# Optimization experiments

Hardware: AMD Instinct MI355X
Metric: run time of the kernel (lower is better)

The kernel has to match this reference:

```python
import jax, jax.numpy as jnp
import numpy as np
from jax import lax

B, L = 2, 1024
D_MODEL, D_STATE, EXPAND, D_CONV = 1024, 16, 2, 4
D_INNER = EXPAND * D_MODEL            # 2048
DT_RANK = (D_MODEL + 15) // 16        # 64


def setup_inputs() -> dict:
    key = jax.random.key(0)
    ks = jax.random.split(key, 8)
    g = lambda k, shape, s=0.02: jax.random.normal(k, shape, dtype=jnp.float32) * s
    # Mamba-style A init: A = -exp(A_log), A_log = log(1..d_state) per channel
    A_log = jnp.log(jnp.broadcast_to(
        jnp.arange(1, D_STATE + 1, dtype=jnp.float32), (D_INNER, D_STATE)))
    return {
        "x": jax.random.normal(ks[0], (B, L, D_MODEL), dtype=jnp.float32),
        "W_in": g(ks[1], (D_MODEL, 2 * D_INNER)),
        "conv_w": g(ks[2], (D_INNER, D_CONV), 0.1),
        "conv_b": jnp.zeros((D_INNER,), jnp.float32),
        "W_x": g(ks[3], (D_INNER, DT_RANK + 2 * D_STATE)),
        "W_dt": g(ks[4], (DT_RANK, D_INNER)),
        "b_dt": g(ks[5], (D_INNER,), 0.1),
        "A_log": A_log,
        "D_skip": jnp.ones((D_INNER,), jnp.float32),
        "W_out": g(ks[6], (D_INNER, D_MODEL)),
    }


def reference(x, W_in, conv_w, conv_b, W_x, W_dt, b_dt, A_log, D_skip, W_out):
    # in_proj -> (u, z): [B, L, D_INNER] each
    xz = x @ W_in
    u, z = xz[..., :D_INNER], xz[..., D_INNER:]

    # causal depthwise conv1d, kernel D_CONV (small fixed loop over taps)
    up = jnp.pad(u, ((0, 0), (D_CONV - 1, 0), (0, 0)))
    u = sum(up[:, k:k + L, :] * conv_w[:, k] for k in range(D_CONV)) + conv_b
    u = jax.nn.silu(u)

    # input-dependent dt, B, C
    x_dbl = u @ W_x                                    # [B, L, dt_rank + 2N]
    dt = x_dbl[..., :DT_RANK]
    Bm = x_dbl[..., DT_RANK:DT_RANK + D_STATE]         # [B, L, N]
    Cm = x_dbl[..., DT_RANK + D_STATE:]                # [B, L, N]
    delta = jax.nn.softplus(dt @ W_dt + b_dt)          # [B, L, D]

    A = -jnp.exp(A_log)                                # [D, N]
    deltaA = jnp.exp(jnp.einsum('bld,dn->bldn', delta, A))   # [B, L, D, N]
    dBu = (delta * u)[..., None] * Bm[:, :, None, :]          # [B, L, D, N]

    def step(h, inp):
        dA_t, dBu_t, c_t = inp                         # [B,D,N],[B,D,N],[B,N]
        h = dA_t * h + dBu_t
        y_t = jnp.einsum('bdn,bn->bd', h, c_t)
        return h, y_t

    h0 = jnp.zeros((B, D_INNER, D_STATE), x.dtype)
    _, ys = lax.scan(step, h0,
                     (deltaA.transpose(1, 0, 2, 3),
                      dBu.transpose(1, 0, 2, 3),
                      Cm.transpose(1, 0, 2)))
    y = ys.transpose(1, 0, 2) + u * D_skip             # [B, L, D_INNER]
    y = y * jax.nn.silu(z)                             # gated output
    return y @ W_out                                   # [B, L, D_MODEL]
```

## Files before the change

### kernel.cpp

```cpp
#include <hip/hip_runtime.h>


typedef unsigned short u16;
typedef unsigned int   u32;

#define B_SZ 2
#define L_SZ 1024
#define DM   1024
#define DI   2048
#define DS   16
#define DTR  64
#define NXD  96
#define NCHUNK 32
#define CL   32
#define KSPLIT 8
#define KC     256

typedef __bf16 bf16x8 __attribute__((ext_vector_type(8)));
typedef float  f32x4  __attribute__((ext_vector_type(4)));

__device__ __forceinline__ u16 f2bf(float f) {
    u32 x = __float_as_uint(f);
    x += 0x7fffu + ((x >> 16) & 1u);
    return (u16)(x >> 16);
}
__device__ __forceinline__ float bf2f(u16 v) {
    return __uint_as_float(((u32)v) << 16);
}

__device__ __forceinline__ void gld_lds16(const u16* g, u16* l) {
    __builtin_amdgcn_global_load_lds(
        (const __attribute__((address_space(1))) u32*)g,
        (__attribute__((address_space(3))) u32*)l, 16, 0, 0);
}

__device__ __forceinline__ void wg_barrier() {
    __asm__ volatile("" ::: "memory");
    __builtin_amdgcn_s_barrier();
    __asm__ volatile("" ::: "memory");
}
#define WAIT_VM12() __builtin_amdgcn_s_waitcnt(0xF7C)
#define WAIT_VM9()  __builtin_amdgcn_s_waitcnt(0xF79)
#define WAIT_VM8()  __builtin_amdgcn_s_waitcnt(0xF78)
#define WAIT_VM6()  __builtin_amdgcn_s_waitcnt(0xF76)
#define WAIT_VM4()  __builtin_amdgcn_s_waitcnt(0xF74)
#define WAIT_VM3()  __builtin_amdgcn_s_waitcnt(0xF73)
#define WAIT_VM0()  __builtin_amdgcn_s_waitcnt(0xF70)

__global__ __launch_bounds__(256) void gemm128p(
    const u16* __restrict__ A, const u16* __restrict__ BT,
    float* __restrict__ Cf, u16* __restrict__ Cb,
    int M, int N, int K, int op)
{
    __shared__ u16 As[4][128 * 32];
    __shared__ u16 Bs[4][128 * 32];

    const int tid  = threadIdx.x;
    const int wave = tid >> 6;
    const int lane = tid & 63;
    const int q    = lane >> 4;
    const int r16  = lane & 15;
    const int wm   = (wave & 1) * 64;
    const int wn   = (wave >> 1) * 64;
    const int m0   = blockIdx.y * 128;
    const int n0   = blockIdx.x * 128;

    const u16* gA0 = A  + (size_t)(m0 + (tid >> 2))      * K + (tid & 3) * 8;
    const u16* gA1 = A  + (size_t)(m0 + 64 + (tid >> 2)) * K + (tid & 3) * 8;
    const u16* gB0 = BT + (size_t)(n0 + (tid >> 2))      * K + (tid & 3) * 8;
    const u16* gB1 = BT + (size_t)(n0 + 64 + (tid >> 2)) * K + (tid & 3) * 8;

    const int niter = K >> 5;
    const int pre = niter < 3 ? niter : 3;
    for (int p = 0; p < pre; ++p) {
        const int k0 = p * 32;
        gld_lds16(gA0 + k0, &As[p][tid * 8]);
        gld_lds16(gA1 + k0, &As[p][2048 + tid * 8]);
        gld_lds16(gB0 + k0, &Bs[p][tid * 8]);
        gld_lds16(gB1 + k0, &Bs[p][2048 + tid * 8]);
    }

    f32x4 acc[4][4];
#pragma unroll
    for (int s = 0; s < 4; ++s)
#pragma unroll
        for (int j = 0; j < 4; ++j) acc[s][j] = (f32x4){0.f, 0.f, 0.f, 0.f};

    for (int it = 0; it < niter; ++it) {
        if (it + 3 < niter) {
            const int k0 = (it + 3) * 32;
            const int bi = (it + 3) & 3;
            gld_lds16(gA0 + k0, &As[bi][tid * 8]);
            gld_lds16(gA1 + k0, &As[bi][2048 + tid * 8]);
            gld_lds16(gB0 + k0, &Bs[bi][tid * 8]);
            gld_lds16(gB1 + k0, &Bs[bi][2048 + tid * 8]);
            WAIT_VM12();
        } else if (it + 2 < niter) {
            WAIT_VM8();
        } else if (it + 1 < niter) {
            WAIT_VM4();
        } else {
            WAIT_VM0();
        }
        wg_barrier();

        const int cur = it & 3;
        bf16x8 af[4], bfr[4];
#pragma unroll
        for (int s = 0; s < 4; ++s)
            af[s] = *(const bf16x8*)(&As[cur][(wm + s * 16 + r16) * 32 + q * 8]);
#pragma unroll
        for (int j = 0; j < 4; ++j)
            bfr[j] = *(const bf16x8*)(&Bs[cur][(wn + j * 16 + r16) * 32 + q * 8]);
#pragma unroll
        for (int s = 0; s < 4; ++s)
#pragma unroll
            for (int j = 0; j < 4; ++j)
                acc[s][j] = __builtin_amdgcn_mfma_f32_16x16x32_bf16(
                    af[s], bfr[j], acc[s][j], 0, 0, 0);

        wg_barrier();
    }

#pragma unroll
    for (int s = 0; s < 4; ++s) {
        const int row0 = m0 + wm + s * 16 + q * 4;
#pragma unroll
        for (int j = 0; j < 4; ++j) {
            const int col = n0 + wn + j * 16 + r16;
            if (op == 2) {
#pragma unroll
                for (int i = 0; i < 4; ++i)
                    Cb[(size_t)(row0 + i) * N + col] = f2bf(acc[s][j][i]);
            } else {
#pragma unroll
                for (int i = 0; i < 4; ++i)
                    Cf[(size_t)(row0 + i) * N + col] = acc[s][j][i];
            }
        }
    }
}

__global__ __launch_bounds__(256) void gemm_out64(
    const u16* __restrict__ A, const u16* __restrict__ BT,
    float* __restrict__ C, int M, int N, int K)
{
    __shared__ u16 As[4][128 * 32];
    __shared__ u16 Bs[4][64 * 32];

    const int tid  = threadIdx.x;
    const int wave = tid >> 6;
    const int lane = tid & 63;
    const int q    = lane >> 4;
    const int r16  = lane & 15;
    const int wm   = (wave & 1) * 64;
    const int wn   = (wave >> 1) * 32;
    const int m0   = blockIdx.y * 128;
    const int n0   = blockIdx.x * 64;

    const u16* gA0 = A  + (size_t)(m0 + (tid >> 2))      * K + (tid & 3) * 8;
    const u16* gA1 = A  + (size_t)(m0 + 64 + (tid >> 2)) * K + (tid & 3) * 8;
    const u16* gB0 = BT + (size_t)(n0 + (tid >> 2))      * K + (tid & 3) * 8;

    const int niter = K >> 5;
    const int pre = niter < 3 ? niter : 3;
    for (int p = 0; p < pre; ++p) {
        const int k0 = p * 32;
        gld_lds16(gA0 + k0, &As[p][tid * 8]);
        gld_lds16(gA1 + k0, &As[p][2048 + tid * 8]);
        gld_lds16(gB0 + k0, &Bs[p][tid * 8]);
    }

    f32x4 acc[4][2];
#pragma unroll
    for (int s = 0; s < 4; ++s)
#pragma unroll
        for (int j = 0; j < 2; ++j) acc[s][j] = (f32x4){0.f, 0.f, 0.f, 0.f};

    for (int it = 0; it < niter; ++it) {
        if (it + 3 < niter) {
            const int k0 = (it + 3) * 32;
            const int bi = (it + 3) & 3;
            gld_lds16(gA0 + k0, &As[bi][tid * 8]);
            gld_lds16(gA1 + k0, &As[bi][2048 + tid * 8]);
            gld_lds16(gB0 + k0, &Bs[bi][tid * 8]);
            WAIT_VM9();
        } else if (it + 2 < niter) {
            WAIT_VM6();
        } else if (it + 1 < niter) {
            WAIT_VM3();
        } else {
            WAIT_VM0();
        }
        wg_barrier();

        const int cur = it & 3;
        bf16x8 af[4], bfr[2];
#pragma unroll
        for (int s = 0; s < 4; ++s)
            af[s] = *(const bf16x8*)(&As[cur][(wm + s * 16 + r16) * 32 + q * 8]);
#pragma unroll
        for (int j = 0; j < 2; ++j)
            bfr[j] = *(const bf16x8*)(&Bs[cur][(wn + j * 16 + r16) * 32 + q * 8]);
#pragma unroll
        for (int s = 0; s < 4; ++s)
#pragma unroll
            for (int j = 0; j < 2; ++j)
                acc[s][j] = __builtin_amdgcn_mfma_f32_16x16x32_bf16(
                    af[s], bfr[j], acc[s][j], 0, 0, 0);

        wg_barrier();
    }

#pragma unroll
    for (int s = 0; s < 4; ++s) {
        const int row0 = m0 + wm + s * 16 + q * 4;
#pragma unroll
        for (int j = 0; j < 2; ++j) {
            const int col = n0 + wn + j * 16 + r16;
#pragma unroll
            for (int i = 0; i < 4; ++i)
                C[(size_t)(row0 + i) * N + col] = acc[s][j][i];
        }
    }
}

__global__ __launch_bounds__(256) void gemm_skinny_atomic(
    const u16* __restrict__ A, const u16* __restrict__ BT,
    float* xdbl, int M, int N, int K)
{
    constexpr int LDT = 40;
    __shared__ u16 As[128 * LDT];
    __shared__ u16 Bs[64 * LDT];

    const int tid  = threadIdx.x;
    const int wave = tid >> 6;
    const int lane = tid & 63;
    const int q    = lane >> 4;
    const int r16  = lane & 15;
    const int m0   = blockIdx.y * 128;
    const int n0   = blockIdx.x * 64;
    const int kcs  = blockIdx.z * KC;
    const int sr   = tid >> 2;
    const int ss   = (tid & 3) * 8;

    f32x4 acc[2][4];
#pragma unroll
    for (int s = 0; s < 2; ++s)
#pragma unroll
        for (int j = 0; j < 4; ++j) acc[s][j] = (f32x4){0.f, 0.f, 0.f, 0.f};

    const int bcol  = n0 + sr;
    const int bcolc = bcol < N ? bcol : N - 1;

    constexpr int NIT = KC / 32;
    uint4 a0 = *(const uint4*)(A + (size_t)(m0 + sr)      * K + kcs + ss);
    uint4 a1 = *(const uint4*)(A + (size_t)(m0 + 64 + sr) * K + kcs + ss);
    uint4 bv = *(const uint4*)(BT + (size_t)bcolc * K + kcs + ss);

    for (int it = 0; it < NIT; ++it) {
        wg_barrier();
        *(uint4*)(As + sr * LDT + ss)        = a0;
        *(uint4*)(As + (64 + sr) * LDT + ss) = a1;
        *(uint4*)(Bs + sr * LDT + ss)        = bv;
        const int kn = (it + 1 < NIT) ? (kcs + (it + 1) * 32) : kcs;
        a0 = *(const uint4*)(A + (size_t)(m0 + sr)      * K + kn + ss);
        a1 = *(const uint4*)(A + (size_t)(m0 + 64 + sr) * K + kn + ss);
        bv = *(const uint4*)(BT + (size_t)bcolc * K + kn + ss);
        __builtin_amdgcn_s_waitcnt(0xF70 | 0x0000);
        __builtin_amdgcn_s_waitcnt(0x070F);
        wg_barrier();

        bf16x8 af[2], bfr[4];
#pragma unroll
        for (int s = 0; s < 2; ++s)
            af[s] = *(const bf16x8*)(As + (wave * 32 + s * 16 + r16) * LDT + q * 8);
#pragma unroll
        for (int j = 0; j < 4; ++j)
            bfr[j] = *(const bf16x8*)(Bs + (j * 16 + r16) * LDT + q * 8);
#pragma unroll
        for (int s = 0; s < 2; ++s)
#pragma unroll
            for (int j = 0; j < 4; ++j)
                acc[s][j] = __builtin_amdgcn_mfma_f32_16x16x32_bf16(
                    af[s], bfr[j], acc[s][j], 0, 0, 0);
    }

#pragma unroll
    for (int s = 0; s < 2; ++s) {
        const int row0 = m0 + wave * 32 + s * 16 + q * 4;
#pragma unroll
        for (int j = 0; j < 4; ++j) {
            const int col = n0 + j * 16 + r16;
            if (col < N) {
#pragma unroll
                for (int i = 0; i < 4; ++i)
                    atomicAdd(&xdbl[(size_t)(row0 + i) * N + col], acc[s][j][i]);
            }
        }
    }
}

__global__ __launch_bounds__(256) void gemm_delta(
    const float* __restrict__ xdbl, const u16* __restrict__ BT,
    const float* __restrict__ bias, float* __restrict__ dlt)
{
    constexpr int LDT = 40;
    __shared__ u16 As[128 * LDT];
    __shared__ u16 Bs[128 * LDT];

    const int tid  = threadIdx.x;
    const int wave = tid >> 6;
    const int lane = tid & 63;
    const int q    = lane >> 4;
    const int r16  = lane & 15;
    const int wm   = (wave & 1) * 64;
    const int wn   = (wave >> 1) * 64;
    const int m0   = blockIdx.y * 128;
    const int n0   = blockIdx.x * 128;
    const int sr   = tid >> 2;
    const int ss   = (tid & 3) * 8;

    f32x4 acc[4][4];
#pragma unroll
    for (int s = 0; s < 4; ++s)
#pragma unroll
        for (int j = 0; j < 4; ++j) acc[s][j] = (f32x4){0.f, 0.f, 0.f, 0.f};

    for (int k0 = 0; k0 < DTR; k0 += 32) {
        __syncthreads();
        f32x4 f0 = *(const f32x4*)(xdbl + (size_t)(m0 + sr) * NXD + k0 + ss);
        f32x4 f1 = *(const f32x4*)(xdbl + (size_t)(m0 + sr) * NXD + k0 + ss + 4);
        f32x4 f2 = *(const f32x4*)(xdbl + (size_t)(m0 + 64 + sr) * NXD + k0 + ss);
        f32x4 f3 = *(const f32x4*)(xdbl + (size_t)(m0 + 64 + sr) * NXD + k0 + ss + 4);
        uint4 bv0 = *(const uint4*)(BT + (size_t)(n0 + sr)      * DTR + k0 + ss);
        uint4 bv1 = *(const uint4*)(BT + (size_t)(n0 + 64 + sr) * DTR + k0 + ss);
        u16* pa0 = As + sr * LDT + ss;
        u16* pa1 = As + (64 + sr) * LDT + ss;
#pragma unroll
        for (int i = 0; i < 4; ++i) { pa0[i] = f2bf(f0[i]); pa0[4 + i] = f2bf(f1[i]); }
#pragma unroll
        for (int i = 0; i < 4; ++i) { pa1[i] = f2bf(f2[i]); pa1[4 + i] = f2bf(f3[i]); }
        *(uint4*)(Bs + sr * LDT + ss)        = bv0;
        *(uint4*)(Bs + (64 + sr) * LDT + ss) = bv1;
        __syncthreads();

        bf16x8 af[4], bfr[4];
#pragma unroll
        for (int s = 0; s < 4; ++s)
            af[s] = *(const bf16x8*)(As + (wm + s * 16 + r16) * LDT + q * 8);
#pragma unroll
        for (int j = 0; j < 4; ++j)
            bfr[j] = *(const bf16x8*)(Bs + (wn + j * 16 + r16) * LDT + q * 8);
#pragma unroll
        for (int s = 0; s < 4; ++s)
#pragma unroll
            for (int j = 0; j < 4; ++j)
                acc[s][j] = __builtin_amdgcn_mfma_f32_16x16x32_bf16(
                    af[s], bfr[j], acc[s][j], 0, 0, 0);
    }

#pragma unroll
    for (int s = 0; s < 4; ++s) {
        const int row0 = m0 + wm + s * 16 + q * 4;
#pragma unroll
        for (int j = 0; j < 4; ++j) {
            const int col = n0 + wn + j * 16 + r16;
            const float bv = bias[col];
#pragma unroll
            for (int i = 0; i < 4; ++i) {
                float v = acc[s][j][i] + bv;
                v = (v > 20.f) ? v : log1pf(__expf(v));
                dlt[(size_t)(row0 + i) * DI + col] = v;
            }
        }
    }
}

__device__ __forceinline__ void tr_tile(
    const float* __restrict__ in, u16* __restrict__ out,
    int R, int C, int tr, int tc, int tid, float (*t)[33])
{
    const int tx = tid & 31, ty = tid >> 5;
    const int r0 = tr * 32, c0 = tc * 32;
#pragma unroll
    for (int i = 0; i < 4; ++i) {
        int r = r0 + ty + i * 8, c = c0 + tx;
        if (r < R && c < C) t[ty + i * 8][tx] = in[(size_t)r * C + c];
    }
    __syncthreads();
#pragma unroll
    for (int i = 0; i < 4; ++i) {
        int oR = c0 + ty + i * 8, oC = r0 + tx;
        if (oR < C && oC < R) out[(size_t)oR * R + oC] = f2bf(t[tx][ty + i * 8]);
    }
}

__global__ __launch_bounds__(256) void prep_kernel(
    const float* __restrict__ x,     u16* __restrict__ xbf,
    const float* __restrict__ W_in,  u16* __restrict__ winT,
    const float* __restrict__ W_out, u16* __restrict__ woutT,
    const float* __restrict__ W_x,   u16* __restrict__ wxT,
    const float* __restrict__ W_dt,  u16* __restrict__ wdtT,
    float* __restrict__ xdbl)
{
    __shared__ float t[32][33];
    const int id  = blockIdx.x;
    const int tid = threadIdx.x;
    if (id < 4096) {
        tr_tile(W_in, winT, 1024, 4096, id >> 7, id & 127, tid, t);
    } else if (id < 6144) {
        int i2 = id - 4096;
        tr_tile(W_out, woutT, 2048, 1024, i2 >> 5, i2 & 31, tid, t);
    } else if (id < 6336) {
        int i3 = id - 6144;
        tr_tile(W_x, wxT, 2048, 96, i3 / 3, i3 % 3, tid, t);
    } else if (id < 6464) {
        int i4 = id - 6336;
        tr_tile(W_dt, wdtT, 64, 2048, i4 >> 6, i4 & 63, tid, t);
    } else if (id < 14656) {
        int i = (id - 6464) * 256 + tid;
        xbf[i] = f2bf(x[i]);
    } else {
        f32x4 z = (f32x4){0.f, 0.f, 0.f, 0.f};
        ((f32x4*)xdbl)[(size_t)(id - 14656) * 256 + tid] = z;
    }
}

__global__ __launch_bounds__(256) void conv_silu_kernel(
    const u16* __restrict__ xzbf, const float* __restrict__ cw,
    const float* __restrict__ cb, u16* __restrict__ ucbf)
{
    const int idx = blockIdx.x * 256 + threadIdx.x;
    const int d   = idx & (DI - 1);
    const int pos = idx >> 11;
    const int l   = pos & (L_SZ - 1);
    float s = cb[d];
#pragma unroll
    for (int k = 0; k < 4; ++k) {
        int ls = l + k - 3;
        if (ls >= 0)
            s = fmaf(bf2f(xzbf[(size_t)(pos + k - 3) * (2 * DI) + d]), cw[d * 4 + k], s);
    }
    float v = s / (1.f + __expf(-s));
    ucbf[idx] = f2bf(v);
}

__global__ __launch_bounds__(256) void scan_pass1(
    const float* __restrict__ delta, const u16* __restrict__ ucbf,
    const float* __restrict__ xdbl, const float* __restrict__ A_log,
    float* __restrict__ hbuf, float* __restrict__ pbuf)
{
    const int c = blockIdx.x;
    const int d = blockIdx.y * 256 + threadIdx.x;
    const int b = blockIdx.z;
    float Av[16], h[16], P[16];
#pragma unroll
    for (int n = 0; n < 16; ++n) {
        Av[n] = -__expf(A_log[d * 16 + n]);
        h[n] = 0.f; P[n] = 1.f;
    }
    const int rowbase = b * L_SZ + c * CL;
    for (int i = 0; i < CL; ++i) {
        const int row = rowbase + i;
        float dlt = delta[(size_t)row * DI + d];
        float uu  = bf2f(ucbf[(size_t)row * DI + d]);
        float du  = dlt * uu;
        const float* xr = xdbl + (size_t)row * NXD;
#pragma unroll
        for (int n = 0; n < 16; ++n) {
            float e = __expf(dlt * Av[n]);
            P[n] *= e;
            h[n] = fmaf(e, h[n], du * xr[DTR + n]);
        }
    }
    size_t base = ((size_t)((b * NCHUNK + c) * DI + d)) * 16;
#pragma unroll
    for (int n = 0; n < 16; ++n) { hbuf[base + n] = h[n]; pbuf[base + n] = P[n]; }
}

__global__ __launch_bounds__(256) void scan_pass2(
    float* __restrict__ hbuf, const float* __restrict__ pbuf)
{
    const int j = blockIdx.x * 256 + threadIdx.x;
    const int b = blockIdx.y;
    float h0 = 0.f;
    for (int cc = 0; cc < NCHUNK; ++cc) {
        size_t o = ((size_t)(b * NCHUNK + cc)) * (DI * 16) + j;
        float hl = hbuf[o];
        float Pl = pbuf[o];
        hbuf[o] = h0;
        h0 = fmaf(Pl, h0, hl);
    }
}

__global__ __launch_bounds__(256) void scan_pass3(
    const float* __restrict__ delta, const u16* __restrict__ ucbf,
    const float* __restrict__ xdbl, const float* __restrict__ A_log,
    const float* __restrict__ hbuf, const u16* __restrict__ xzbf,
    const float* __restrict__ Dskip, u16* __restrict__ ybf)
{
    const int c = blockIdx.x;
    const int d = blockIdx.y * 256 + threadIdx.x;
    const int b = blockIdx.z;
    float Av[16], h[16];
    size_t base = ((size_t)((b * NCHUNK + c) * DI + d)) * 16;
#pragma unroll
    for (int n = 0; n < 16; ++n) {
        Av[n] = -__expf(A_log[d * 16 + n]);
        h[n]  = hbuf[base + n];
    }
    const float Dk = Dskip[d];
    const int rowbase = b * L_SZ + c * CL;
    for (int i = 0; i < CL; ++i) {
        const int row = rowbase + i;
        float dlt = delta[(size_t)row * DI + d];
        float uu  = bf2f(ucbf[(size_t)row * DI + d]);
        float du  = dlt * uu;
        const float* xr = xdbl + (size_t)row * NXD;
        float y = 0.f;
#pragma unroll
        for (int n = 0; n < 16; ++n) {
            float e = __expf(dlt * Av[n]);
            h[n] = fmaf(e, h[n], du * xr[DTR + n]);
            y = fmaf(h[n], xr[DTR + DS + n], y);
        }
        float zz = bf2f(xzbf[(size_t)row * (2 * DI) + DI + d]);
        float yv = fmaf(uu, Dk, y) * (zz / (1.f + __expf(-zz)));
        ybf[(size_t)row * DI + d] = f2bf(yv);
    }
}

constexpr size_t OFF_DELTA   = 0;
constexpr size_t OFF_XDBL    = OFF_DELTA + 4194304;
constexpr size_t OFF_HBUF    = OFF_XDBL  + 196608;
constexpr size_t OFF_PBUF    = OFF_HBUF  + 2097152;
constexpr size_t OFF_F32_END = OFF_PBUF  + 2097152;
constexpr size_t SOFF_XBF   = 0;
constexpr size_t SOFF_WINT  = SOFF_XBF   + 2097152;
constexpr size_t SOFF_XZBF  = SOFF_WINT  + 4194304;
constexpr size_t SOFF_UCBF  = SOFF_XZBF  + 8388608;
constexpr size_t SOFF_WXT   = SOFF_UCBF  + 4194304;
constexpr size_t SOFF_WDTT  = SOFF_WXT   + 196608;
constexpr size_t SOFF_WOUTT = SOFF_WDTT  + 131072;
constexpr size_t SOFF_YBF   = SOFF_WOUTT + 2097152;

extern "C" void kernel_launch(void* const* d_in, const int* in_sizes, int n_in,
                              void* d_out, int out_size, void* d_ws, size_t ws_size,
                              hipStream_t stream)
{
    const float* x     = (const float*)d_in[0];
    const float* W_in  = (const float*)d_in[1];
    const float* cw    = (const float*)d_in[2];
    const float* cb    = (const float*)d_in[3];
    const float* W_x   = (const float*)d_in[4];
    const float* W_dt  = (const float*)d_in[5];
    const float* b_dt  = (const float*)d_in[6];
    const float* A_log = (const float*)d_in[7];
    const float* Dsk   = (const float*)d_in[8];
    const float* W_out = (const float*)d_in[9];
    float* out = (float*)d_out;

    float* wsf   = (float*)d_ws;
    float* dlt   = wsf + OFF_DELTA;
    float* xdbl  = wsf + OFF_XDBL;
    float* hbuf  = wsf + OFF_HBUF;
    float* pbuf  = wsf + OFF_PBUF;
    u16* sb    = (u16*)(wsf + OFF_F32_END);
    u16* xbf   = sb + SOFF_XBF;
    u16* winT  = sb + SOFF_WINT;
    u16* xzbf  = sb + SOFF_XZBF;
    u16* ucbf  = sb + SOFF_UCBF;
    u16* wxT   = sb + SOFF_WXT;
    u16* wdtT  = sb + SOFF_WDTT;
    u16* woutT = sb + SOFF_WOUTT;
    u16* ybf   = sb + SOFF_YBF;

    prep_kernel<<<14848, 256, 0, stream>>>(x, xbf, W_in, winT, W_out, woutT,
                                           W_x, wxT, W_dt, wdtT, xdbl);

    gemm128p<<<dim3(32, 16), 256, 0, stream>>>(
        xbf, winT, nullptr, xzbf, 2048, 4096, 1024, 2);

    conv_silu_kernel<<<(B_SZ * L_SZ * DI) / 256, 256, 0, stream>>>(xzbf, cw, cb, ucbf);

    gemm_skinny_atomic<<<dim3(2, 16, KSPLIT), 256, 0, stream>>>(
        ucbf, wxT, xdbl, 2048, NXD, 2048);

    gemm_delta<<<dim3(16, 16), 256, 0, stream>>>(xdbl, wdtT, b_dt, dlt);

    scan_pass1<<<dim3(NCHUNK, DI / 256, B_SZ), 256, 0, stream>>>(dlt, ucbf, xdbl, A_log, hbuf, pbuf);
    scan_pass2<<<dim3(DI * 16 / 256, B_SZ), 256, 0, stream>>>(hbuf, pbuf);
    scan_pass3<<<dim3(NCHUNK, DI / 256, B_SZ), 256, 0, stream>>>(dlt, ucbf, xdbl, A_log, hbuf, xzbf, Dsk, ybf);

    gemm_out64<<<dim3(16, 16), 256, 0, stream>>>(ybf, woutT, out, 2048, 1024, 2048);
}
```

Measured before the change: 262.9 us.

## Fuse conv, x-proj, delta GEMM and three scan passes into one cooperative kernel

```diff
diff --git a/kernel.cpp b/kernel.cpp
--- a/kernel.cpp
+++ b/kernel.cpp
@@ -1,5 +1,8 @@
 #include <hip/hip_runtime.h>
-
+#include <hip/hip_cooperative_groups.h>
+
+
+namespace cg = cooperative_groups;
 
 typedef unsigned short u16;
 typedef unsigned int   u32;
@@ -46,6 +49,7 @@
 #define WAIT_VM4()  __builtin_amdgcn_s_waitcnt(0xF74)
 #define WAIT_VM3()  __builtin_amdgcn_s_waitcnt(0xF73)
 #define WAIT_VM0()  __builtin_amdgcn_s_waitcnt(0xF70)
+#define WAIT_LGKM0() __builtin_amdgcn_s_waitcnt(0x070F)
 
 __global__ __launch_bounds__(256) void gemm128p(
     const u16* __restrict__ A, const u16* __restrict__ BT,
@@ -221,158 +225,6 @@
 #pragma unroll
             for (int i = 0; i < 4; ++i)
                 C[(size_t)(row0 + i) * N + col] = acc[s][j][i];
-        }
-    }
-}
-
-__global__ __launch_bounds__(256) void gemm_skinny_atomic(
-    const u16* __restrict__ A, const u16* __restrict__ BT,
-    float* xdbl, int M, int N, int K)
-{
-    constexpr int LDT = 40;
-    __shared__ u16 As[128 * LDT];
-    __shared__ u16 Bs[64 * LDT];
-
-    const int tid  = threadIdx.x;
-    const int wave = tid >> 6;
-    const int lane = tid & 63;
-    const int q    = lane >> 4;
-    const int r16  = lane & 15;
-    const int m0   = blockIdx.y * 128;
-    const int n0   = blockIdx.x * 64;
-    const int kcs  = blockIdx.z * KC;
-    const int sr   = tid >> 2;
-    const int ss   = (tid & 3) * 8;
-
-    f32x4 acc[2][4];
-#pragma unroll
-    for (int s = 0; s < 2; ++s)
-#pragma unroll
-        for (int j = 0; j < 4; ++j) acc[s][j] = (f32x4){0.f, 0.f, 0.f, 0.f};
-
-    const int bcol  = n0 + sr;
-    const int bcolc = bcol < N ? bcol : N - 1;
-
-    constexpr int NIT = KC / 32;
-    uint4 a0 = *(const uint4*)(A + (size_t)(m0 + sr)      * K + kcs + ss);
-    uint4 a1 = *(const uint4*)(A + (size_t)(m0 + 64 + sr) * K + kcs + ss);
-    uint4 bv = *(const uint4*)(BT + (size_t)bcolc * K + kcs + ss);
-
-    for (int it = 0; it < NIT; ++it) {
-        wg_barrier();
-        *(uint4*)(As + sr * LDT + ss)        = a0;
-        *(uint4*)(As + (64 + sr) * LDT + ss) = a1;
-        *(uint4*)(Bs + sr * LDT + ss)        = bv;
-        const int kn = (it + 1 < NIT) ? (kcs + (it + 1) * 32) : kcs;
-        a0 = *(const uint4*)(A + (size_t)(m0 + sr)      * K + kn + ss);
-        a1 = *(const uint4*)(A + (size_t)(m0 + 64 + sr) * K + kn + ss);
-        bv = *(const uint4*)(BT + (size_t)bcolc * K + kn + ss);
-        __builtin_amdgcn_s_waitcnt(0xF70 | 0x0000);
-        __builtin_amdgcn_s_waitcnt(0x070F);
-        wg_barrier();
-
-        bf16x8 af[2], bfr[4];
-#pragma unroll
-        for (int s = 0; s < 2; ++s)
-            af[s] = *(const bf16x8*)(As + (wave * 32 + s * 16 + r16) * LDT + q * 8);
-#pragma unroll
-        for (int j = 0; j < 4; ++j)
-            bfr[j] = *(const bf16x8*)(Bs + (j * 16 + r16) * LDT + q * 8);
-#pragma unroll
-        for (int s = 0; s < 2; ++s)
-#pragma unroll
-            for (int j = 0; j < 4; ++j)
-                acc[s][j] = __builtin_amdgcn_mfma_f32_16x16x32_bf16(
-                    af[s], bfr[j], acc[s][j], 0, 0, 0);
-    }
-
-#pragma unroll
-    for (int s = 0; s < 2; ++s) {
-        const int row0 = m0 + wave * 32 + s * 16 + q * 4;
-#pragma unroll
-        for (int j = 0; j < 4; ++j) {
-            const int col = n0 + j * 16 + r16;
-            if (col < N) {
-#pragma unroll
-                for (int i = 0; i < 4; ++i)
-                    atomicAdd(&xdbl[(size_t)(row0 + i) * N + col], acc[s][j][i]);
-            }
-        }
-    }
-}
-
-__global__ __launch_bounds__(256) void gemm_delta(
-    const float* __restrict__ xdbl, const u16* __restrict__ BT,
-    const float* __restrict__ bias, float* __restrict__ dlt)
-{
-    constexpr int LDT = 40;
-    __shared__ u16 As[128 * LDT];
-    __shared__ u16 Bs[128 * LDT];
-
-    const int tid  = threadIdx.x;
-    const int wave = tid >> 6;
-    const int lane = tid & 63;
-    const int q    = lane >> 4;
-    const int r16  = lane & 15;
-    const int wm   = (wave & 1) * 64;
-    const int wn   = (wave >> 1) * 64;
-    const int m0   = blockIdx.y * 128;
-    const int n0   = blockIdx.x * 128;
-    const int sr   = tid >> 2;
-    const int ss   = (tid & 3) * 8;
-
-    f32x4 acc[4][4];
-#pragma unroll
-    for (int s = 0; s < 4; ++s)
-#pragma unroll
-        for (int j = 0; j < 4; ++j) acc[s][j] = (f32x4){0.f, 0.f, 0.f, 0.f};
-
-    for (int k0 = 0; k0 < DTR; k0 += 32) {
-        __syncthreads();
-        f32x4 f0 = *(const f32x4*)(xdbl + (size_t)(m0 + sr) * NXD + k0 + ss);
-        f32x4 f1 = *(const f32x4*)(xdbl + (size_t)(m0 + sr) * NXD + k0 + ss + 4);
-        f32x4 f2 = *(const f32x4*)(xdbl + (size_t)(m0 + 64 + sr) * NXD + k0 + ss);
-        f32x4 f3 = *(const f32x4*)(xdbl + (size_t)(m0 + 64 + sr) * NXD + k0 + ss + 4);
-        uint4 bv0 = *(const uint4*)(BT + (size_t)(n0 + sr)      * DTR + k0 + ss);
-        uint4 bv1 = *(const uint4*)(BT + (size_t)(n0 + 64 + sr) * DTR + k0 + ss);
-        u16* pa0 = As + sr * LDT + ss;
-        u16* pa1 = As + (64 + sr) * LDT + ss;
-#pragma unroll
-        for (int i = 0; i < 4; ++i) { pa0[i] = f2bf(f0[i]); pa0[4 + i] = f2bf(f1[i]); }
-#pragma unroll
-        for (int i = 0; i < 4; ++i) { pa1[i] = f2bf(f2[i]); pa1[4 + i] = f2bf(f3[i]); }
-        *(uint4*)(Bs + sr * LDT + ss)        = bv0;
-        *(uint4*)(Bs + (64 + sr) * LDT + ss) = bv1;
-        __syncthreads();
-
-        bf16x8 af[4], bfr[4];
-#pragma unroll
-        for (int s = 0; s < 4; ++s)
-            af[s] = *(const bf16x8*)(As + (wm + s * 16 + r16) * LDT + q * 8);
-#pragma unroll
-        for (int j = 0; j < 4; ++j)
-            bfr[j] = *(const bf16x8*)(Bs + (wn + j * 16 + r16) * LDT + q * 8);
-#pragma unroll
-        for (int s = 0; s < 4; ++s)
-#pragma unroll
-            for (int j = 0; j < 4; ++j)
-                acc[s][j] = __builtin_amdgcn_mfma_f32_16x16x32_bf16(
-                    af[s], bfr[j], acc[s][j], 0, 0, 0);
-    }
-
-#pragma unroll
-    for (int s = 0; s < 4; ++s) {
-        const int row0 = m0 + wm + s * 16 + q * 4;
-#pragma unroll
-        for (int j = 0; j < 4; ++j) {
-            const int col = n0 + wn + j * 16 + r16;
-            const float bv = bias[col];
-#pragma unroll
-            for (int i = 0; i < 4; ++i) {
-                float v = acc[s][j][i] + bv;
-                v = (v > 20.f) ? v : log1pf(__expf(v));
-                dlt[(size_t)(row0 + i) * DI + col] = v;
-            }
         }
     }
 }
@@ -427,107 +279,249 @@
     }
 }
 
-__global__ __launch_bounds__(256) void conv_silu_kernel(
+__global__ __launch_bounds__(256, 2) void mega_kernel(
     const u16* __restrict__ xzbf, const float* __restrict__ cw,
-    const float* __restrict__ cb, u16* __restrict__ ucbf)
+    const float* __restrict__ cb, u16* __restrict__ ucbf,
+    const u16* __restrict__ wxT, float* __restrict__ xdbl,
+    const u16* __restrict__ wdtT, const float* __restrict__ b_dt,
+    float* __restrict__ dlt,
+    const float* __restrict__ A_log, const float* __restrict__ Dsk,
+    float* __restrict__ hbuf, float* __restrict__ pbuf,
+    u16* __restrict__ ybf)
 {
-    const int idx = blockIdx.x * 256 + threadIdx.x;
-    const int d   = idx & (DI - 1);
-    const int pos = idx >> 11;
-    const int l   = pos & (L_SZ - 1);
-    float s = cb[d];
-#pragma unroll
-    for (int k = 0; k < 4; ++k) {
-        int ls = l + k - 3;
-        if (ls >= 0)
-            s = fmaf(bf2f(xzbf[(size_t)(pos + k - 3) * (2 * DI) + d]), cw[d * 4 + k], s);
-    }
-    float v = s / (1.f + __expf(-s));
-    ucbf[idx] = f2bf(v);
-}
-
-__global__ __launch_bounds__(256) void scan_pass1(
-    const float* __restrict__ delta, const u16* __restrict__ ucbf,
-    const float* __restrict__ xdbl, const float* __restrict__ A_log,
-    float* __restrict__ hbuf, float* __restrict__ pbuf)
-{
-    const int c = blockIdx.x;
-    const int d = blockIdx.y * 256 + threadIdx.x;
-    const int b = blockIdx.z;
-    float Av[16], h[16], P[16];
-#pragma unroll
-    for (int n = 0; n < 16; ++n) {
-        Av[n] = -__expf(A_log[d * 16 + n]);
-        h[n] = 0.f; P[n] = 1.f;
-    }
-    const int rowbase = b * L_SZ + c * CL;
-    for (int i = 0; i < CL; ++i) {
-        const int row = rowbase + i;
-        float dlt = delta[(size_t)row * DI + d];
-        float uu  = bf2f(ucbf[(size_t)row * DI + d]);
-        float du  = dlt * uu;
-        const float* xr = xdbl + (size_t)row * NXD;
+    cg::grid_group grid = cg::this_grid();
+    const int bid = blockIdx.x;
+    const int tid = threadIdx.x;
+
+    constexpr int LDT = 40;
+    __shared__ u16 As[128 * LDT];
+    __shared__ u16 Bs[64 * LDT];
+
+    for (int idx = bid * 256 + tid; idx < B_SZ * L_SZ * DI; idx += 512 * 256) {
+        const int d   = idx & (DI - 1);
+        const int pos = idx >> 11;
+        const int l   = pos & (L_SZ - 1);
+        float s = cb[d];
+#pragma unroll
+        for (int k = 0; k < 4; ++k) {
+            int ls = l + k - 3;
+            if (ls >= 0)
+                s = fmaf(bf2f(xzbf[(size_t)(pos + k - 3) * (2 * DI) + d]), cw[d * 4 + k], s);
+        }
+        float v = s / (1.f + __expf(-s));
+        ucbf[idx] = f2bf(v);
+    }
+    grid.sync();
+
+    if (bid < 256) {
+        const int wave = tid >> 6, lane = tid & 63;
+        const int q = lane >> 4, r16 = lane & 15;
+        const int n0  = (bid & 1) * 64;
+        const int m0  = ((bid >> 1) & 15) * 128;
+        const int kcs = (bid >> 5) * KC;
+        const int sr  = tid >> 2, ss = (tid & 3) * 8;
+
+        f32x4 acc[2][4];
+#pragma unroll
+        for (int s = 0; s < 2; ++s)
+#pragma unroll
+            for (int j = 0; j < 4; ++j) acc[s][j] = (f32x4){0.f, 0.f, 0.f, 0.f};
+
+        const int bcol  = n0 + sr;
+        const int bcolc = bcol < NXD ? bcol : NXD - 1;
+
+        constexpr int NIT = KC / 32;
+        uint4 a0 = *(const uint4*)(ucbf + (size_t)(m0 + sr)      * DI + kcs + ss);
+        uint4 a1 = *(const uint4*)(ucbf + (size_t)(m0 + 64 + sr) * DI + kcs + ss);
+        uint4 bv = *(const uint4*)(wxT + (size_t)bcolc * DI + kcs + ss);
+
+        for (int it = 0; it < NIT; ++it) {
+            wg_barrier();
+            *(uint4*)(As + sr * LDT + ss)        = a0;
+            *(uint4*)(As + (64 + sr) * LDT + ss) = a1;
+            *(uint4*)(Bs + sr * LDT + ss)        = bv;
+            const int kn = (it + 1 < NIT) ? (kcs + (it + 1) * 32) : kcs;
+            a0 = *(const uint4*)(ucbf + (size_t)(m0 + sr)      * DI + kn + ss);
+            a1 = *(const uint4*)(ucbf + (size_t)(m0 + 64 + sr) * DI + kn + ss);
+            bv = *(const uint4*)(wxT + (size_t)bcolc * DI + kn + ss);
+            WAIT_LGKM0();
+            wg_barrier();
+
+            bf16x8 af[2], bfr[4];
+#pragma unroll
+            for (int s = 0; s < 2; ++s)
+                af[s] = *(const bf16x8*)(As + (wave * 32 + s * 16 + r16) * LDT + q * 8);
+#pragma unroll
+            for (int j = 0; j < 4; ++j)
+                bfr[j] = *(const bf16x8*)(Bs + (j * 16 + r16) * LDT + q * 8);
+#pragma unroll
+            for (int s = 0; s < 2; ++s)
+#pragma unroll
+                for (int j = 0; j < 4; ++j)
+                    acc[s][j] = __builtin_amdgcn_mfma_f32_16x16x32_bf16(
+                        af[s], bfr[j], acc[s][j], 0, 0, 0);
+        }
+
+#pragma unroll
+        for (int s = 0; s < 2; ++s) {
+            const int row0 = m0 + wave * 32 + s * 16 + q * 4;
+#pragma unroll
+            for (int j = 0; j < 4; ++j) {
+                const int col = n0 + j * 16 + r16;
+                if (col < NXD) {
+#pragma unroll
+                    for (int i = 0; i < 4; ++i)
+                        atomicAdd(&xdbl[(size_t)(row0 + i) * NXD + col], acc[s][j][i]);
+                }
+            }
+        }
+    }
+    grid.sync();
+
+    {
+        const int wave = tid >> 6, lane = tid & 63;
+        const int q = lane >> 4, r16 = lane & 15;
+        const int wm = (wave & 1) * 64, wn = (wave >> 1) * 32;
+        const int n0 = (bid & 31) * 64;
+        const int m0 = (bid >> 5) * 128;
+        const int sr = tid >> 2, ss = (tid & 3) * 8;
+
+        f32x4 acc[4][2];
+#pragma unroll
+        for (int s = 0; s < 4; ++s)
+#pragma unroll
+            for (int j = 0; j < 2; ++j) acc[s][j] = (f32x4){0.f, 0.f, 0.f, 0.f};
+
+        for (int k0 = 0; k0 < DTR; k0 += 32) {
+            __syncthreads();
+            f32x4 f0 = *(const f32x4*)(xdbl + (size_t)(m0 + sr) * NXD + k0 + ss);
+            f32x4 f1 = *(const f32x4*)(xdbl + (size_t)(m0 + sr) * NXD + k0 + ss + 4);
+            f32x4 f2 = *(const f32x4*)(xdbl + (size_t)(m0 + 64 + sr) * NXD + k0 + ss);
+            f32x4 f3 = *(const f32x4*)(xdbl + (size_t)(m0 + 64 + sr) * NXD + k0 + ss + 4);
+            uint4 bv0 = *(const uint4*)(wdtT + (size_t)(n0 + sr) * DTR + k0 + ss);
+            u16* pa0 = As + sr * LDT + ss;
+            u16* pa1 = As + (64 + sr) * LDT + ss;
+#pragma unroll
+            for (int i = 0; i < 4; ++i) { pa0[i] = f2bf(f0[i]); pa0[4 + i] = f2bf(f1[i]); }
+#pragma unroll
+            for (int i = 0; i < 4; ++i) { pa1[i] = f2bf(f2[i]); pa1[4 + i] = f2bf(f3[i]); }
+            *(uint4*)(Bs + sr * LDT + ss) = bv0;
+            __syncthreads();
+
+            bf16x8 af[4], bfr[2];
+#pragma unroll
+            for (int s = 0; s < 4; ++s)
+                af[s] = *(const bf16x8*)(As + (wm + s * 16 + r16) * LDT + q * 8);
+#pragma unroll
+            for (int j = 0; j < 2; ++j)
+                bfr[j] = *(const bf16x8*)(Bs + (wn + j * 16 + r16) * LDT + q * 8);
+#pragma unroll
+            for (int s = 0; s < 4; ++s)
+#pragma unroll
+                for (int j = 0; j < 2; ++j)
+                    acc[s][j] = __builtin_amdgcn_mfma_f32_16x16x32_bf16(
+                        af[s], bfr[j], acc[s][j], 0, 0, 0);
+        }
+
+#pragma unroll
+        for (int s = 0; s < 4; ++s) {
+            const int row0 = m0 + wm + s * 16 + q * 4;
+#pragma unroll
+            for (int j = 0; j < 2; ++j) {
+                const int col = n0 + wn + j * 16 + r16;
+                const float bv = b_dt[col];
+#pragma unroll
+                for (int i = 0; i < 4; ++i) {
+                    float v = acc[s][j][i] + bv;
+                    v = (v > 20.f) ? v : log1pf(__expf(v));
+                    dlt[(size_t)(row0 + i) * DI + col] = v;
+                }
+            }
+        }
+    }
+    grid.sync();
+
+    {
+        const int c = bid & 31;
+        const int r = bid >> 5;
+        const int g = r & 7;
+        const int b = r >> 3;
+        const int d = g * 256 + tid;
+        float Av[16], h[16], P[16];
 #pragma unroll
         for (int n = 0; n < 16; ++n) {
-            float e = __expf(dlt * Av[n]);
-            P[n] *= e;
-            h[n] = fmaf(e, h[n], du * xr[DTR + n]);
-        }
-    }
-    size_t base = ((size_t)((b * NCHUNK + c) * DI + d)) * 16;
-#pragma unroll
-    for (int n = 0; n < 16; ++n) { hbuf[base + n] = h[n]; pbuf[base + n] = P[n]; }
-}
-
-__global__ __launch_bounds__(256) void scan_pass2(
-    float* __restrict__ hbuf, const float* __restrict__ pbuf)
-{
-    const int j = blockIdx.x * 256 + threadIdx.x;
-    const int b = blockIdx.y;
-    float h0 = 0.f;
-    for (int cc = 0; cc < NCHUNK; ++cc) {
-        size_t o = ((size_t)(b * NCHUNK + cc)) * (DI * 16) + j;
-        float hl = hbuf[o];
-        float Pl = pbuf[o];
-        hbuf[o] = h0;
-        h0 = fmaf(Pl, h0, hl);
-    }
-}
-
-__global__ __launch_bounds__(256) void scan_pass3(
-    const float* __restrict__ delta, const u16* __restrict__ ucbf,
-    const float* __restrict__ xdbl, const float* __restrict__ A_log,
-    const float* __restrict__ hbuf, const u16* __restrict__ xzbf,
-    const float* __restrict__ Dskip, u16* __restrict__ ybf)
-{
-    const int c = blockIdx.x;
-    const int d = blockIdx.y * 256 + threadIdx.x;
-    const int b = blockIdx.z;
-    float Av[16], h[16];
-    size_t base = ((size_t)((b * NCHUNK + c) * DI + d)) * 16;
-#pragma unroll
-    for (int n = 0; n < 16; ++n) {
-        Av[n] = -__expf(A_log[d * 16 + n]);
-        h[n]  = hbuf[base + n];
-    }
-    const float Dk = Dskip[d];
-    const int rowbase = b * L_SZ + c * CL;
-    for (int i = 0; i < CL; ++i) {
-        const int row = rowbase + i;
-        float dlt = delta[(size_t)row * DI + d];
-        float uu  = bf2f(ucbf[(size_t)row * DI + d]);
-        float du  = dlt * uu;
-        const float* xr = xdbl + (size_t)row * NXD;
-        float y = 0.f;
+            Av[n] = -__expf(A_log[d * 16 + n]);
+            h[n] = 0.f; P[n] = 1.f;
+        }
+        const int rowbase = b * L_SZ + c * CL;
+        for (int i = 0; i < CL; ++i) {
+            const int row = rowbase + i;
+            float dv = dlt[(size_t)row * DI + d];
+            float uu = bf2f(ucbf[(size_t)row * DI + d]);
+            float du = dv * uu;
+            const float* xr = xdbl + (size_t)row * NXD;
+#pragma unroll
+            for (int n = 0; n < 16; ++n) {
+                float e = __expf(dv * Av[n]);
+                P[n] *= e;
+                h[n] = fmaf(e, h[n], du * xr[DTR + n]);
+            }
+        }
+        size_t base = ((size_t)((b * NCHUNK + c) * DI + d)) * 16;
+#pragma unroll
+        for (int n = 0; n < 16; ++n) { hbuf[base + n] = h[n]; pbuf[base + n] = P[n]; }
+    }
+    grid.sync();
+
+    {
+        const int tidg = bid * 256 + tid;
+        if (tidg < 2 * DI * 16) {
+            const int b = tidg >> 15;
+            const int j = tidg & (DI * 16 - 1);
+            float h0 = 0.f;
+            for (int cc = 0; cc < NCHUNK; ++cc) {
+                size_t o = ((size_t)(b * NCHUNK + cc)) * (DI * 16) + j;
+                float hl = hbuf[o];
+                float Pl = pbuf[o];
+                hbuf[o] = h0;
+                h0 = fmaf(Pl, h0, hl);
+            }
+        }
+    }
+    grid.sync();
+
+    {
+        const int c = bid & 31;
+        const int r = bid >> 5;
+        const int g = r & 7;
+        const int b = r >> 3;
+        const int d = g * 256 + tid;
+        float Av[16], h[16];
+        size_t base = ((size_t)((b * NCHUNK + c) * DI + d)) * 16;
 #pragma unroll
         for (int n = 0; n < 16; ++n) {
-            float e = __expf(dlt * Av[n]);
-            h[n] = fmaf(e, h[n], du * xr[DTR + n]);
-            y = fmaf(h[n], xr[DTR + DS + n], y);
-        }
-        float zz = bf2f(xzbf[(size_t)row * (2 * DI) + DI + d]);
-        float yv = fmaf(uu, Dk, y) * (zz / (1.f + __expf(-zz)));
-        ybf[(size_t)row * DI + d] = f2bf(yv);
+            Av[n] = -__expf(A_log[d * 16 + n]);
+            h[n]  = hbuf[base + n];
+        }
+        const float Dk = Dsk[d];
+        const int rowbase = b * L_SZ + c * CL;
+        for (int i = 0; i < CL; ++i) {
+            const int row = rowbase + i;
+            float dv = dlt[(size_t)row * DI + d];
+            float uu = bf2f(ucbf[(size_t)row * DI + d]);
+            float du = dv * uu;
+            const float* xr = xdbl + (size_t)row * NXD;
+            float y = 0.f;
+#pragma unroll
+            for (int n = 0; n < 16; ++n) {
+                float e = __expf(dv * Av[n]);
+                h[n] = fmaf(e, h[n], du * xr[DTR + n]);
+                y = fmaf(h[n], xr[DTR + DS + n], y);
+            }
+            float zz = bf2f(xzbf[(size_t)row * (2 * DI) + DI + d]);
+            float yv = fmaf(uu, Dk, y) * (zz / (1.f + __expf(-zz)));
+            ybf[(size_t)row * DI + d] = f2bf(yv);
+        }
     }
 }
 
@@ -582,16 +576,17 @@
     gemm128p<<<dim3(32, 16), 256, 0, stream>>>(
         xbf, winT, nullptr, xzbf, 2048, 4096, 1024, 2);
 
-    conv_silu_kernel<<<(B_SZ * L_SZ * DI) / 256, 256, 0, stream>>>(xzbf, cw, cb, ucbf);
-
-    gemm_skinny_atomic<<<dim3(2, 16, KSPLIT), 256, 0, stream>>>(
-        ucbf, wxT, xdbl, 2048, NXD, 2048);
-
-    gemm_delta<<<dim3(16, 16), 256, 0, stream>>>(xdbl, wdtT, b_dt, dlt);
-
-    scan_pass1<<<dim3(NCHUNK, DI / 256, B_SZ), 256, 0, stream>>>(dlt, ucbf, xdbl, A_log, hbuf, pbuf);
-    scan_pass2<<<dim3(DI * 16 / 256, B_SZ), 256, 0, stream>>>(hbuf, pbuf);
-    scan_pass3<<<dim3(NCHUNK, DI / 256, B_SZ), 256, 0, stream>>>(dlt, ucbf, xdbl, A_log, hbuf, xzbf, Dsk, ybf);
+    {
+        void* margs[] = {
+            (void*)&xzbf, (void*)&cw, (void*)&cb, (void*)&ucbf,
+            (void*)&wxT,  (void*)&xdbl,
+            (void*)&wdtT, (void*)&b_dt, (void*)&dlt,
+            (void*)&A_log, (void*)&Dsk,
+            (void*)&hbuf, (void*)&pbuf, (void*)&ybf
+        };
+        hipLaunchCooperativeKernel((const void*)mega_kernel,
+                                   dim3(512), dim3(256), margs, 0, stream);
+    }
 
     gemm_out64<<<dim3(16, 16), 256, 0, stream>>>(ybf, woutT, out, 2048, 1024, 2048);
 }
```

After: 574.1 us. +118.4%, slower.

## Fuse causal conv and SiLU into the skinny x_proj GEMM prologue

Applied to the files above, without the earlier changes.

```diff
diff --git a/kernel.cpp b/kernel.cpp
--- a/kernel.cpp
+++ b/kernel.cpp
@@ -225,9 +225,10 @@
     }
 }
 
-__global__ __launch_bounds__(256) void gemm_skinny_atomic(
-    const u16* __restrict__ A, const u16* __restrict__ BT,
-    float* xdbl, int M, int N, int K)
+__global__ __launch_bounds__(256) void gemm_skinny_conv(
+    const u16* __restrict__ xzbf, const float* __restrict__ cw,
+    const float* __restrict__ cb, const u16* __restrict__ BT,
+    float* xdbl, u16* __restrict__ ucbf)
 {
     constexpr int LDT = 40;
     __shared__ u16 As[128 * LDT];
@@ -251,25 +252,58 @@
         for (int j = 0; j < 4; ++j) acc[s][j] = (f32x4){0.f, 0.f, 0.f, 0.f};
 
     const int bcol  = n0 + sr;
-    const int bcolc = bcol < N ? bcol : N - 1;
+    const int bcolc = bcol < NXD ? bcol : NXD - 1;
 
     constexpr int NIT = KC / 32;
-    uint4 a0 = *(const uint4*)(A + (size_t)(m0 + sr)      * K + kcs + ss);
-    uint4 a1 = *(const uint4*)(A + (size_t)(m0 + 64 + sr) * K + kcs + ss);
-    uint4 bv = *(const uint4*)(BT + (size_t)bcolc * K + kcs + ss);
-
     for (int it = 0; it < NIT; ++it) {
-        wg_barrier();
-        *(uint4*)(As + sr * LDT + ss)        = a0;
-        *(uint4*)(As + (64 + sr) * LDT + ss) = a1;
-        *(uint4*)(Bs + sr * LDT + ss)        = bv;
-        const int kn = (it + 1 < NIT) ? (kcs + (it + 1) * 32) : kcs;
-        a0 = *(const uint4*)(A + (size_t)(m0 + sr)      * K + kn + ss);
-        a1 = *(const uint4*)(A + (size_t)(m0 + 64 + sr) * K + kn + ss);
-        bv = *(const uint4*)(BT + (size_t)bcolc * K + kn + ss);
-        __builtin_amdgcn_s_waitcnt(0xF70 | 0x0000);
-        __builtin_amdgcn_s_waitcnt(0x070F);
-        wg_barrier();
+        const int c = kcs + it * 32 + ss;
+        __syncthreads();
+
+        f32x4 cwv[8];
+        float cbv[8];
+#pragma unroll
+        for (int j = 0; j < 8; ++j) {
+            cwv[j] = *(const f32x4*)(cw + (size_t)(c + j) * 4);
+            cbv[j] = cb[c + j];
+        }
+
+        uint4 ua[2];
+#pragma unroll
+        for (int rsel = 0; rsel < 2; ++rsel) {
+            const int r = m0 + rsel * 64 + sr;
+            const int l = r & (L_SZ - 1);
+            float s8[8];
+#pragma unroll
+            for (int j = 0; j < 8; ++j) s8[j] = cbv[j];
+#pragma unroll
+            for (int k = 0; k < 4; ++k) {
+                if (l + k - 3 >= 0) {
+                    uint4 xv = *(const uint4*)(xzbf + (size_t)(r + k - 3) * (2 * DI) + c);
+                    const u16* xp = (const u16*)&xv;
+#pragma unroll
+                    for (int j = 0; j < 8; ++j) {
+                        const float w = (k == 0) ? cwv[j].x : (k == 1) ? cwv[j].y
+                                       : (k == 2) ? cwv[j].z : cwv[j].w;
+                        s8[j] = fmaf(bf2f(xp[j]), w, s8[j]);
+                    }
+                }
+            }
+            u16* up = (u16*)&ua[rsel];
+#pragma unroll
+            for (int j = 0; j < 8; ++j) {
+                float v = s8[j] / (1.f + __expf(-s8[j]));
+                up[j] = f2bf(v);
+            }
+        }
+        *(uint4*)(As + sr * LDT + ss)        = ua[0];
+        *(uint4*)(As + (64 + sr) * LDT + ss) = ua[1];
+        if (n0 == 0) {
+            *(uint4*)(ucbf + (size_t)(m0 + sr) * DI + c)      = ua[0];
+            *(uint4*)(ucbf + (size_t)(m0 + 64 + sr) * DI + c) = ua[1];
+        }
+        *(uint4*)(Bs + sr * LDT + ss) =
+            *(const uint4*)(BT + (size_t)bcolc * DI + kcs + it * 32 + ss);
+        __syncthreads();
 
         bf16x8 af[2], bfr[4];
 #pragma unroll
@@ -292,10 +326,10 @@
 #pragma unroll
         for (int j = 0; j < 4; ++j) {
             const int col = n0 + j * 16 + r16;
-            if (col < N) {
+            if (col < NXD) {
 #pragma unroll
                 for (int i = 0; i < 4; ++i)
-                    atomicAdd(&xdbl[(size_t)(row0 + i) * N + col], acc[s][j][i]);
+                    atomicAdd(&xdbl[(size_t)(row0 + i) * NXD + col], acc[s][j][i]);
             }
         }
     }
@@ -427,25 +461,6 @@
     }
 }
 
-__global__ __launch_bounds__(256) void conv_silu_kernel(
-    const u16* __restrict__ xzbf, const float* __restrict__ cw,
-    const float* __restrict__ cb, u16* __restrict__ ucbf)
-{
-    const int idx = blockIdx.x * 256 + threadIdx.x;
-    const int d   = idx & (DI - 1);
-    const int pos = idx >> 11;
-    const int l   = pos & (L_SZ - 1);
-    float s = cb[d];
-#pragma unroll
-    for (int k = 0; k < 4; ++k) {
-        int ls = l + k - 3;
-        if (ls >= 0)
-            s = fmaf(bf2f(xzbf[(size_t)(pos + k - 3) * (2 * DI) + d]), cw[d * 4 + k], s);
-    }
-    float v = s / (1.f + __expf(-s));
-    ucbf[idx] = f2bf(v);
-}
-
 __global__ __launch_bounds__(256) void scan_pass1(
     const float* __restrict__ delta, const u16* __restrict__ ucbf,
     const float* __restrict__ xdbl, const float* __restrict__ A_log,
@@ -582,10 +597,8 @@
     gemm128p<<<dim3(32, 16), 256, 0, stream>>>(
         xbf, winT, nullptr, xzbf, 2048, 4096, 1024, 2);
 
-    conv_silu_kernel<<<(B_SZ * L_SZ * DI) / 256, 256, 0, stream>>>(xzbf, cw, cb, ucbf);
-
-    gemm_skinny_atomic<<<dim3(2, 16, KSPLIT), 256, 0, stream>>>(
-        ucbf, wxT, xdbl, 2048, NXD, 2048);
+    gemm_skinny_conv<<<dim3(2, 16, KSPLIT), 256, 0, stream>>>(
+        xzbf, cw, cb, wxT, xdbl, ucbf);
 
     gemm_delta<<<dim3(16, 16), 256, 0, stream>>>(xdbl, wdtT, b_dt, dlt);
 
```

New measurement: 265.0 us. No clear change (+0.8%).
